# Kernel optimization log

Hardware: AMD Instinct MI355X
Metric: run time of the kernel (lower is better)

Reference implementation:

```python
import jax, jax.numpy as jnp
import numpy as np
from jax import lax

B_IDX = 0  # label_vocab['B']
E_IDX = 1  # label_vocab['E']
NEG = -10000.0


def setup_inputs() -> dict:
    key = jax.random.key(0)
    k1, k2 = jax.random.split(key)
    B, T, L = 256, 512, 64
    X = jax.random.normal(k1, (B, T, L), dtype=jnp.float32)
    transition = jax.random.normal(k2, (L, L), dtype=jnp.float32)
    # __init__ masking: no transitions out of 'E', none into 'B'
    transition = transition.at[E_IDX, :].set(NEG)
    transition = transition.at[:, B_IDX].set(NEG)
    return {"X": X, "transition": transition}


def reference(X, transition):
    # CRF forward (alpha) recursion, vectorized over the tag dimension and
    # batched; recurrence over timesteps carried by lax.scan.
    B, T, L = X.shape
    init_alpha = jnp.full((B, L), NEG, dtype=X.dtype).at[:, B_IDX].set(0.0)

    def step(alpha, x_t):
        # alpha: [B, L] (prev tag), x_t: [B, L] (emission for next tag)
        # next_var[b, prev, nxt] = alpha[b, prev] + transition[prev, nxt] + x_t[b, nxt]
        next_var = alpha[:, :, None] + transition[None, :, :] + x_t[:, None, :]
        new_alpha = jax.nn.logsumexp(next_var, axis=1)  # reduce over prev tag
        return new_alpha, None

    X_tbl = jnp.moveaxis(X, 1, 0)  # [T, B, L]
    final_alpha, _ = lax.scan(step, init_alpha, X_tbl)
    return final_alpha  # [B, L]
```

## Files before the change

### kernel.cpp

```cpp
#include <hip/hip_runtime.h>

#define LTAG 64
#define NEGV -10000.0f
#define L2E 1.4426950408889634f
#define LN2 0.6931471805599453f

typedef float vfloat2 __attribute__((ext_vector_type(2)));

__device__ __forceinline__ float exp2_fast(float x) { return __builtin_amdgcn_exp2f(x); }
__device__ __forceinline__ float log2_fast(float x) { return __builtin_amdgcn_logf(x); }

__device__ __forceinline__ float readlane_f(float v, int lane) {
    return __int_as_float(__builtin_amdgcn_readlane(__float_as_int(v), lane));
}

__global__ __launch_bounds__(64) void crf_forward_kernel(
    const float* __restrict__ X, const float* __restrict__ trans,
    float* __restrict__ out, int T) {
    const int lane = threadIdx.x;
    const int b = blockIdx.x;
    const float* xb = X + (size_t)b * T * LTAG + lane;

    __shared__ __align__(16) float e_sh[LTAG];

    float etrL[32];
    vfloat2 etrH[16];
    float c2 = -3.0e38f;
#pragma unroll
    for (int p = 0; p < 32; ++p) {
        etrL[p] = trans[p * LTAG + lane] * L2E;
        c2 = fmaxf(c2, etrL[p]);
    }
#pragma unroll
    for (int i = 0; i < 16; ++i) {
        const float t0 = trans[(32 + 2 * i) * LTAG + lane] * L2E;
        const float t1 = trans[(33 + 2 * i) * LTAG + lane] * L2E;
        c2 = fmaxf(c2, fmaxf(t0, t1));
        etrH[i].x = t0;
        etrH[i].y = t1;
    }
#pragma unroll
    for (int p = 0; p < 32; ++p) etrL[p] = exp2_fast(etrL[p] - c2);
#pragma unroll
    for (int i = 0; i < 16; ++i) {
        etrH[i].x = exp2_fast(etrH[i].x - c2);
        etrH[i].y = exp2_fast(etrH[i].y - c2);
    }

    float A = (lane == 0) ? 1.0f : 0.0f;
    float SH = 0.0f;
    float sB = 1.0f, xB = 0.0f, shB = 0.0f;

    float xr[4];
#pragma unroll
    for (int i = 0; i < 4; ++i) xr[i] = xb[(size_t)i * LTAG];

    e_sh[lane] = A;

#define SUBSTEP(u, PF_STMT)                                                   \
    {                                                                         \
        const float xcur = xr[u];                                             \
        PF_STMT;                                                              \
               \
        const float g = exp2_fast(fmaf(xcur, L2E, c2));                       \
                    \
        float4 ev[8];                                                         \
        _Pragma("unroll") for (int i = 0; i < 8; ++i)                         \
            ev[i] = *(const float4*)(e_sh + 32 + 4 * i);                      \
                    \
        float ub[32];                                                         \
        _Pragma("unroll") for (int p = 0; p < 32; ++p)                        \
            ub[p] = readlane_f(A, p);                                         \
        float s0 = 0.f, s1 = 0.f, s2 = 0.f, s3 = 0.f;                         \
        _Pragma("unroll") for (int p = 0; p < 32; p += 4) {                   \
            s0 = fmaf(ub[p + 0], etrL[p + 0], s0);                            \
            s1 = fmaf(ub[p + 1], etrL[p + 1], s1);                            \
            s2 = fmaf(ub[p + 2], etrL[p + 2], s2);                            \
            s3 = fmaf(ub[p + 3], etrL[p + 3], s3);                            \
        }                                                                     \
                            \
        vfloat2 h0 = {0.f, 0.f}, h1 = {0.f, 0.f};                             \
        _Pragma("unroll") for (int i = 0; i < 8; ++i) {                       \
            const vfloat2 ea = {ev[i].x, ev[i].y};                            \
            const vfloat2 eb = {ev[i].z, ev[i].w};                            \
            h0 = __builtin_elementwise_fma(ea, etrH[2 * i + 0], h0);          \
            h1 = __builtin_elementwise_fma(eb, etrH[2 * i + 1], h1);          \
        }                                                                     \
        const vfloat2 hh = h0 + h1;                                           \
        const float s = ((s0 + s1) + (s2 + s3)) + (hh.x + hh.y);              \
        sB = s; xB = xcur; shB = SH;     \
        A = s * g;                                                            \
        if (u == 3) {                                                         \
                   \
                   \
            float mm = fmaxf(readlane_f(A, 2), readlane_f(A, 19));            \
            mm = fmaxf(mm, readlane_f(A, 28));                                \
            mm = fmaxf(mm, fmaxf(readlane_f(A, 37), readlane_f(A, 53)));      \
            int eb2 = (__float_as_int(mm) >> 23) & 0xff;                      \
            eb2 = eb2 < 1 ? 1 : eb2;                                          \
            A *= __int_as_float((254 - eb2) << 23);  \
            SH += (float)(eb2 - 127);                                         \
        }                                                                     \
        e_sh[lane] = A;           \
    }

    const float* xp = xb + 4 * (size_t)LTAG;
    int t = 0;
    for (; t + 8 <= T; t += 4) {
        SUBSTEP(0, xr[0] = xp[0 * LTAG]);
        SUBSTEP(1, xr[1] = xp[1 * LTAG]);
        SUBSTEP(2, xr[2] = xp[2 * LTAG]);
        SUBSTEP(3, xr[3] = xp[3 * LTAG]);
        xp += 4 * LTAG;
    }
    for (; t < T; t += 4) {
        SUBSTEP(0, );
        SUBSTEP(1, );
        SUBSTEP(2, );
        SUBSTEP(3, );
    }
#undef SUBSTEP

    float res;
    if (lane == 0) {
        res = (log2_fast(sB) + fmaf(xB, L2E, c2) + shB) * LN2;
    } else {
        res = (log2_fast(A) + SH) * LN2;
    }
    out[b * LTAG + lane] = res;
}

extern "C" void kernel_launch(void* const* d_in, const int* in_sizes, int n_in,
                              void* d_out, int out_size, void* d_ws, size_t ws_size,
                              hipStream_t stream) {
    const float* X = (const float*)d_in[0];
    const float* trans = (const float*)d_in[1];
    float* out = (float*)d_out;

    const int B = out_size / LTAG;
    const int T = in_sizes[0] / (B * LTAG);

    crf_forward_kernel<<<B, LTAG, 0, stream>>>(X, trans, out, T);
}
```

Measured before the change: 192.8 us.

## Split per-step prev-tag reduction across four waves with LDS partial sums

Each batch row now runs four waves instead of one. Each wave handles 16 of the 64 previous tags through readlane FMAs, writes a partial sum to a double-buffered LDS array, and after a workgroup barrier every wave sums the four partials. This cuts the serial FMA and readlane chain per timestep to a quarter. In exchange it adds an s_barrier and LDS round trip at every timestep, and all waves redundantly load X and compute the rescaling.

```diff
diff --git a/kernel.cpp b/kernel.cpp
--- a/kernel.cpp
+++ b/kernel.cpp
@@ -1,11 +1,9 @@
 #include <hip/hip_runtime.h>
 
 #define LTAG 64
-#define NEGV -10000.0f
+#define WAVES 4
 #define L2E 1.4426950408889634f
 #define LN2 0.6931471805599453f
-
-typedef float vfloat2 __attribute__((ext_vector_type(2)));
 
 __device__ __forceinline__ float exp2_fast(float x) { return __builtin_amdgcn_exp2f(x); }
 __device__ __forceinline__ float log2_fast(float x) { return __builtin_amdgcn_logf(x); }
@@ -14,38 +12,24 @@
     return __int_as_float(__builtin_amdgcn_readlane(__float_as_int(v), lane));
 }
 
-__global__ __launch_bounds__(64) void crf_forward_kernel(
+__global__ __launch_bounds__(WAVES * 64) void crf_forward_kernel(
     const float* __restrict__ X, const float* __restrict__ trans,
     float* __restrict__ out, int T) {
-    const int lane = threadIdx.x;
+    const int tid = threadIdx.x;
+    const int lane = tid & 63;
+    const int wid = __builtin_amdgcn_readfirstlane(tid >> 6);
     const int b = blockIdx.x;
     const float* xb = X + (size_t)b * T * LTAG + lane;
 
-    __shared__ __align__(16) float e_sh[LTAG];
+    __shared__ __align__(16) float part[2][WAVES * LTAG];
 
-    float etrL[32];
-    vfloat2 etrH[16];
     float c2 = -3.0e38f;
 #pragma unroll
-    for (int p = 0; p < 32; ++p) {
-        etrL[p] = trans[p * LTAG + lane] * L2E;
-        c2 = fmaxf(c2, etrL[p]);
-    }
+    for (int p = 0; p < LTAG; ++p) c2 = fmaxf(c2, trans[p * LTAG + lane] * L2E);
+    float etr16[16];
 #pragma unroll
-    for (int i = 0; i < 16; ++i) {
-        const float t0 = trans[(32 + 2 * i) * LTAG + lane] * L2E;
-        const float t1 = trans[(33 + 2 * i) * LTAG + lane] * L2E;
-        c2 = fmaxf(c2, fmaxf(t0, t1));
-        etrH[i].x = t0;
-        etrH[i].y = t1;
-    }
-#pragma unroll
-    for (int p = 0; p < 32; ++p) etrL[p] = exp2_fast(etrL[p] - c2);
-#pragma unroll
-    for (int i = 0; i < 16; ++i) {
-        etrH[i].x = exp2_fast(etrH[i].x - c2);
-        etrH[i].y = exp2_fast(etrH[i].y - c2);
-    }
+    for (int i = 0; i < 16; ++i)
+        etr16[i] = exp2_fast(trans[(wid * 16 + i) * LTAG + lane] * L2E - c2);
 
     float A = (lane == 0) ? 1.0f : 0.0f;
     float SH = 0.0f;
@@ -55,44 +39,38 @@
 #pragma unroll
     for (int i = 0; i < 4; ++i) xr[i] = xb[(size_t)i * LTAG];
 
-    e_sh[lane] = A;
+    const int pbase = wid * 16;
+    int buf = 0;
 
 #define SUBSTEP(u, PF_STMT)                                                   \
     {                                                                         \
         const float xcur = xr[u];                                             \
         PF_STMT;                                                              \
-               \
+              \
         const float g = exp2_fast(fmaf(xcur, L2E, c2));                       \
-                    \
-        float4 ev[8];                                                         \
-        _Pragma("unroll") for (int i = 0; i < 8; ++i)                         \
-            ev[i] = *(const float4*)(e_sh + 32 + 4 * i);                      \
-                    \
-        float ub[32];                                                         \
-        _Pragma("unroll") for (int p = 0; p < 32; ++p)                        \
-            ub[p] = readlane_f(A, p);                                         \
-        float s0 = 0.f, s1 = 0.f, s2 = 0.f, s3 = 0.f;                         \
-        _Pragma("unroll") for (int p = 0; p < 32; p += 4) {                   \
-            s0 = fmaf(ub[p + 0], etrL[p + 0], s0);                            \
-            s1 = fmaf(ub[p + 1], etrL[p + 1], s1);                            \
-            s2 = fmaf(ub[p + 2], etrL[p + 2], s2);                            \
-            s3 = fmaf(ub[p + 3], etrL[p + 3], s3);                            \
+            \
+        float ub[16];                                                         \
+        _Pragma("unroll") for (int i = 0; i < 16; ++i)                        \
+            ub[i] = readlane_f(A, pbase + i);                                 \
+        float q0 = 0.f, q1 = 0.f, q2 = 0.f, q3 = 0.f;                         \
+        _Pragma("unroll") for (int i = 0; i < 16; i += 4) {                   \
+            q0 = fmaf(ub[i + 0], etr16[i + 0], q0);                           \
+            q1 = fmaf(ub[i + 1], etr16[i + 1], q1);                           \
+            q2 = fmaf(ub[i + 2], etr16[i + 2], q2);                           \
+            q3 = fmaf(ub[i + 3], etr16[i + 3], q3);                           \
         }                                                                     \
-                            \
-        vfloat2 h0 = {0.f, 0.f}, h1 = {0.f, 0.f};                             \
-        _Pragma("unroll") for (int i = 0; i < 8; ++i) {                       \
-            const vfloat2 ea = {ev[i].x, ev[i].y};                            \
-            const vfloat2 eb = {ev[i].z, ev[i].w};                            \
-            h0 = __builtin_elementwise_fma(ea, etrH[2 * i + 0], h0);          \
-            h1 = __builtin_elementwise_fma(eb, etrH[2 * i + 1], h1);          \
-        }                                                                     \
-        const vfloat2 hh = h0 + h1;                                           \
-        const float s = ((s0 + s1) + (s2 + s3)) + (hh.x + hh.y);              \
-        sB = s; xB = xcur; shB = SH;     \
+        part[buf][wid * LTAG + lane] = (q0 + q1) + (q2 + q3);                 \
+         \
+        asm volatile("s_waitcnt lgkmcnt(0)\n\ts_barrier" ::: "memory");       \
+           \
+        const float s = (part[buf][lane] + part[buf][LTAG + lane]) +          \
+                        (part[buf][2 * LTAG + lane] + part[buf][3 * LTAG + lane]); \
+        buf ^= 1;                                                             \
+        sB = s; xB = xcur; shB = SH;        \
         A = s * g;                                                            \
         if (u == 3) {                                                         \
                    \
-                   \
+                  \
             float mm = fmaxf(readlane_f(A, 2), readlane_f(A, 19));            \
             mm = fmaxf(mm, readlane_f(A, 28));                                \
             mm = fmaxf(mm, fmaxf(readlane_f(A, 37), readlane_f(A, 53)));      \
@@ -101,7 +79,6 @@
             A *= __int_as_float((254 - eb2) << 23);  \
             SH += (float)(eb2 - 127);                                         \
         }                                                                     \
-        e_sh[lane] = A;           \
     }
 
     const float* xp = xb + 4 * (size_t)LTAG;
@@ -127,7 +104,7 @@
     } else {
         res = (log2_fast(A) + SH) * LN2;
     }
-    out[b * LTAG + lane] = res;
+    if (wid == 0) out[b * LTAG + lane] = res;
 }
 
 extern "C" void kernel_launch(void* const* d_in, const int* in_sizes, int n_in,
@@ -140,5 +117,5 @@
     const int B = out_size / LTAG;
     const int T = in_sizes[0] / (B * LTAG);
 
-    crf_forward_kernel<<<B, LTAG, 0, stream>>>(X, trans, out, T);
+    crf_forward_kernel<<<B, WAVES * 64, 0, stream>>>(X, trans, out, T);
 }
```

After: 177.1 us. 1.09x faster.
